# Optimization experiments

Measured on AMD Instinct MI355X. Metric: run time of the kernel, lower is better.

The kernel has to match this reference:

```python
import jax, jax.numpy as jnp
import numpy as np

D_MODEL = 768
NUM_HEADS = 12
D_K = D_MODEL // NUM_HEADS


def setup_inputs() -> dict:
    key = jax.random.key(0)
    ks = jax.random.split(key, 11)
    B, S = 2, 2048
    sc = 1.0 / np.sqrt(D_MODEL)
    return {
        "q": jax.random.normal(ks[0], (B, S, D_MODEL), jnp.float32),
        "k": jax.random.normal(ks[1], (B, S, D_MODEL), jnp.float32),
        "v": jax.random.normal(ks[2], (B, S, D_MODEL), jnp.float32),
        "w_q": jax.random.normal(ks[3], (D_MODEL, D_MODEL), jnp.float32) * sc,
        "b_q": jnp.zeros((D_MODEL,), jnp.float32),
        "w_k": jax.random.normal(ks[4], (D_MODEL, D_MODEL), jnp.float32) * sc,
        "b_k": jnp.zeros((D_MODEL,), jnp.float32),
        "w_v": jax.random.normal(ks[5], (D_MODEL, D_MODEL), jnp.float32) * sc,
        "b_v": jnp.zeros((D_MODEL,), jnp.float32),
        "w_o": jax.random.normal(ks[6], (D_MODEL, D_MODEL), jnp.float32) * sc,
        "b_o": jnp.zeros((D_MODEL,), jnp.float32),
    }


def _split_heads(x, B):
    # [B, S, D] -> [B, H, S, d_k]
    return x.reshape(B, -1, NUM_HEADS, D_K).transpose(0, 2, 1, 3)


def reference(q, k, v, w_q, b_q, w_k, b_k, w_v, b_v, w_o, b_o):
    B = q.shape[0]
    # torch nn.Linear: y = x @ W.T + b; weights stored [out, in]
    qh = _split_heads(q @ w_q.T + b_q, B)
    kh = _split_heads(k @ w_k.T + b_k, B)
    vh = _split_heads(v @ w_v.T + b_v, B)
    scores = jnp.einsum("bhsd,bhtd->bhst", qh, kh) / jnp.sqrt(jnp.float32(D_K))
    attn = jax.nn.softmax(scores, axis=-1)
    ctx = jnp.einsum("bhst,bhtd->bhsd", attn, vh)
    ctx = ctx.transpose(0, 2, 1, 3).reshape(B, -1, D_MODEL)
    return ctx @ w_o.T + b_o
```

## Files before the change

### kernel.cpp

```cpp
#include <hip/hip_runtime.h>
#include <cstdint>


#define S_LEN 2048
#define NHEAD 12
#define DMODEL 768

typedef short s16x8 __attribute__((ext_vector_type(8)));
typedef float f32x4 __attribute__((ext_vector_type(4)));

#define MFMA16(a, b, c) __builtin_amdgcn_mfma_f32_16x16x32_bf16((a), (b), (c), 0, 0, 0)

__device__ __forceinline__ unsigned int pk_bf16(float a, float b) {
  unsigned int ua = __float_as_uint(a), ub = __float_as_uint(b);
  ua = (ua + 0x7FFFu + ((ua >> 16) & 1u)) >> 16;
  ub = (ub + 0x7FFFu + ((ub >> 16) & 1u)) >> 16;
  return ua | (ub << 16);
}
__device__ __forceinline__ short bf16r(float a) {
  unsigned int ua = __float_as_uint(a);
  return (short)((ua + 0x7FFFu + ((ua >> 16) & 1u)) >> 16);
}
__device__ __forceinline__ unsigned int pk_trunc(float a, float b) {
  return __builtin_amdgcn_perm(__float_as_uint(b), __float_as_uint(a), 0x07060302u);
}
__device__ __forceinline__ float bf16_floor(float a) {
  return __uint_as_float(__float_as_uint(a) & 0xFFFF0000u);
}

__global__ __launch_bounds__(256)
void convert_w(const float* __restrict__ w0, const float* __restrict__ w1,
               const float* __restrict__ w2, const float* __restrict__ w3,
               short* __restrict__ o0, short* __restrict__ o1,
               short* __restrict__ o2, short* __restrict__ o3) {
  const float* src = (blockIdx.y == 0) ? w0 : (blockIdx.y == 1) ? w1
                   : (blockIdx.y == 2) ? w2 : w3;
  short* dst = (blockIdx.y == 0) ? o0 : (blockIdx.y == 1) ? o1
             : (blockIdx.y == 2) ? o2 : o3;
  const long i = ((long)blockIdx.x * 256 + threadIdx.x) * 4;
  float4 f = *(const float4*)(src + i);
  uint2 u;
  u.x = pk_bf16(f.x, f.y);
  u.y = pk_bf16(f.z, f.w);
  *(uint2*)(dst + i) = u;
}

template <bool ABF>
__device__ __forceinline__ void gemm64x128db(const void* __restrict__ Av,
                                             const short* __restrict__ Bv,
                                             int m0, int n0, f32x4 (&acc)[2][4],
                                             short* Alds, short* Blds) {
  constexpr int K = 768;
  constexpr int NIT = K / 32;
  const int tid  = threadIdx.x;
  const int lane = tid & 63;
  const int w    = tid >> 6;
  const int g    = lane >> 4;
  const int c    = lane & 15;
  const int wm   = (w & 1) * 32;
  const int wn   = (w >> 1) * 64;
  const int ar   = tid >> 2, ac = (tid & 3) * 8;
  const int br   = tid >> 1, bc = (tid & 1) * 16;

#pragma unroll
  for (int i = 0; i < 2; ++i)
#pragma unroll
    for (int j = 0; j < 4; ++j) acc[i][j] = (f32x4){0.f, 0.f, 0.f, 0.f};

  short* A0 = Alds;            short* B0 = Blds;
  short* A1 = Alds + 64 * 40;  short* B1 = Blds + 128 * 40;

  float4 rafA0, rafA1, rafB0, rafB1;
  uint4  rabA, rabB;
  uint4  rbA0, rbA1, rbB0, rbB1;

  auto fetchA = [&](int kt) {
    if (ABF) {
      rabA = *(const uint4*)((const short*)Av + (long)(m0 + ar) * K + kt + ac);
    } else {
      const float* Ap = (const float*)Av + (long)(m0 + ar) * K + kt + ac;
      rafA0 = ((const float4*)Ap)[0];
      rafA1 = ((const float4*)Ap)[1];
    }
    const short* Bp = Bv + (long)(n0 + br) * K + kt + bc;
    rbA0 = *(const uint4*)Bp;
    rbA1 = *(const uint4*)(Bp + 8);
  };
  auto fetchB = [&](int kt) {
    if (ABF) {
      rabB = *(const uint4*)((const short*)Av + (long)(m0 + ar) * K + kt + ac);
    } else {
      const float* Ap = (const float*)Av + (long)(m0 + ar) * K + kt + ac;
      rafB0 = ((const float4*)Ap)[0];
      rafB1 = ((const float4*)Ap)[1];
    }
    const short* Bp = Bv + (long)(n0 + br) * K + kt + bc;
    rbB0 = *(const uint4*)Bp;
    rbB1 = *(const uint4*)(Bp + 8);
  };
  auto storeA = [&](short* Ab, short* Bb) {
    if (ABF) {
      *(uint4*)&Ab[ar * 40 + ac] = rabA;
    } else {
      uint4 u;
      u.x = pk_bf16(rafA0.x, rafA0.y); u.y = pk_bf16(rafA0.z, rafA0.w);
      u.z = pk_bf16(rafA1.x, rafA1.y); u.w = pk_bf16(rafA1.z, rafA1.w);
      *(uint4*)&Ab[ar * 40 + ac] = u;
    }
    *(uint4*)&Bb[br * 40 + bc]     = rbA0;
    *(uint4*)&Bb[br * 40 + bc + 8] = rbA1;
  };
  auto storeB = [&](short* Ab, short* Bb) {
    if (ABF) {
      *(uint4*)&Ab[ar * 40 + ac] = rabB;
    } else {
      uint4 u;
      u.x = pk_bf16(rafB0.x, rafB0.y); u.y = pk_bf16(rafB0.z, rafB0.w);
      u.z = pk_bf16(rafB1.x, rafB1.y); u.w = pk_bf16(rafB1.z, rafB1.w);
      *(uint4*)&Ab[ar * 40 + ac] = u;
    }
    *(uint4*)&Bb[br * 40 + bc]     = rbB0;
    *(uint4*)&Bb[br * 40 + bc + 8] = rbB1;
  };
  auto compute = [&](const short* Ab, const short* Bb) {
    s16x8 af[2], bf[4];
#pragma unroll
    for (int mb = 0; mb < 2; ++mb)
      af[mb] = *(const s16x8*)&Ab[(wm + mb * 16 + c) * 40 + g * 8];
#pragma unroll
    for (int nb = 0; nb < 4; ++nb)
      bf[nb] = *(const s16x8*)&Bb[(wn + nb * 16 + c) * 40 + g * 8];
#pragma unroll
    for (int mb = 0; mb < 2; ++mb)
#pragma unroll
      for (int nb = 0; nb < 4; ++nb)
        acc[mb][nb] = MFMA16(af[mb], bf[nb], acc[mb][nb]);
  };

  fetchA(0);
  fetchB(32);
  storeA(A0, B0);
  for (int j = 0; j < NIT / 2; ++j) {
    __syncthreads();
    fetchA((2 * j + 2 < NIT) ? (2 * j + 2) * 32 : 0);
    compute(A0, B0);
    storeB(A1, B1);
    __syncthreads();
    fetchB((2 * j + 3 < NIT) ? (2 * j + 3) * 32 : 0);
    compute(A1, B1);
    storeA(A0, B0);
  }
}

__global__ __launch_bounds__(256)
void qkv_kernel(const float* __restrict__ q, const float* __restrict__ k,
                const float* __restrict__ v,
                const short* __restrict__ wq, const short* __restrict__ wk,
                const short* __restrict__ wv,
                const float* __restrict__ bq, const float* __restrict__ bk,
                const float* __restrict__ bv,
                short* __restrict__ qh, short* __restrict__ kh,
                short* __restrict__ vt) {
  __shared__ short Alds[2 * 64 * 40];
  __shared__ short Blds[2 * 128 * 40];

  const int L   = blockIdx.x;
  const int xcd = L & 7;
  const int i   = L >> 3;
  const int nt  = i % 6;
  const int pl  = xcd * 24 + i / 6;
  const int z   = pl >> 6;
  const int mt  = pl & 63;
  const int m0  = mt * 64;
  const int n0  = nt * 128;

  const float* A = (z == 0) ? q : (z == 1) ? k : v;
  const short* B = (z == 0) ? wq : (z == 1) ? wk : wv;
  const float* bias = (z == 0) ? bq : (z == 1) ? bk : bv;

  f32x4 acc[2][4];
  gemm64x128db<false>(A, B, m0, n0, acc, Alds, Blds);

  const int lane = threadIdx.x & 63, w = threadIdx.x >> 6;
  const int g = lane >> 4, c = lane & 15;
  const int wm = (w & 1) * 32, wn = (w >> 1) * 64;

  if (z < 2) {
    short* outp = z ? kh : qh;
    const float scale = z ? 1.0f : 0.18033688011112042f;
#pragma unroll
    for (int mb = 0; mb < 2; ++mb) {
#pragma unroll
      for (int nb = 0; nb < 4; ++nb) {
        const int n = n0 + wn + nb * 16 + c;
        const float bvv = bias[n];
        const int hh = n >> 6, d = n & 63;
#pragma unroll
        for (int r = 0; r < 4; ++r) {
          const int m = m0 + wm + mb * 16 + g * 4 + r;
          const int b = m >> 11, s = m & 2047;
          const float val = (acc[mb][nb][r] + bvv) * scale;
          outp[(((long)(b * NHEAD + hh) * S_LEN + s) << 6) + d] = bf16r(val);
        }
      }
    }
  } else {
#pragma unroll
    for (int mb = 0; mb < 2; ++mb) {
#pragma unroll
      for (int nb = 0; nb < 4; ++nb) {
        const int n = n0 + wn + nb * 16 + c;
        const float bvv = bias[n];
        const int hh = n >> 6, d = n & 63;
        const int m_base = m0 + wm + mb * 16 + g * 4;
        const int b = m_base >> 11, t = m_base & 2047;
        uint2 ov;
        ov.x = pk_bf16(acc[mb][nb][0] + bvv, acc[mb][nb][1] + bvv);
        ov.y = pk_bf16(acc[mb][nb][2] + bvv, acc[mb][nb][3] + bvv);
        *(uint2*)(vt + ((long)(b * NHEAD + hh) * 64 + d) * S_LEN + t) = ov;
      }
    }
  }
}

__global__ __launch_bounds__(256)
void o_kernel(const short* __restrict__ ctx, const short* __restrict__ wo,
              const float* __restrict__ bo, float* __restrict__ out) {
  __shared__ short Alds[2 * 64 * 40];
  __shared__ short Blds[2 * 128 * 40];

  const int L   = blockIdx.x;
  const int xcd = L & 7;
  const int i   = L >> 3;
  const int nt  = i % 6;
  const int mt  = xcd * 8 + i / 6;
  const int m0  = mt * 64;
  const int n0  = nt * 128;

  f32x4 acc[2][4];
  gemm64x128db<true>(ctx, wo, m0, n0, acc, Alds, Blds);

  const int lane = threadIdx.x & 63, w = threadIdx.x >> 6;
  const int g = lane >> 4, c = lane & 15;
  const int wm = (w & 1) * 32, wn = (w >> 1) * 64;
#pragma unroll
  for (int mb = 0; mb < 2; ++mb) {
#pragma unroll
    for (int nb = 0; nb < 4; ++nb) {
      const int n = n0 + wn + nb * 16 + c;
      const float bvv = bo[n];
#pragma unroll
      for (int r = 0; r < 4; ++r) {
        const int m = m0 + wm + mb * 16 + g * 4 + r;
        out[(long)m * DMODEL + n] = acc[mb][nb][r] + bvv;
      }
    }
  }
}

__global__ __launch_bounds__(256)
void attn_kernel(const short* __restrict__ Qh, const short* __restrict__ Kh,
                 const short* __restrict__ Vt, short* __restrict__ Ctx) {
  __shared__ short kbuf[2][64 * 64];
  __shared__ short vbuf[2][64 * 64];
  __shared__ short pbuf[4][16 * 64];

  const int tid  = threadIdx.x;
  const int lane = tid & 63;
  const int w    = tid >> 6;
  const int g    = lane >> 4;
  const int c    = lane & 15;
  const int bh   = blockIdx.y;
  const int qs0  = blockIdx.x * 64;
  const long base = (long)bh * S_LEN * 64;
  const short* Qb = Qh + base;
  const short* Kb = Kh + base;
  const short* Vb = Vt + base;

  const long qrow = (long)(qs0 + w * 16 + c) * 64;
  const s16x8 qf0 = *(const s16x8*)(Qb + qrow + g * 8);
  const s16x8 qf1 = *(const s16x8*)(Qb + qrow + 32 + g * 8);

  f32x4 co[4];
#pragma unroll
  for (int i = 0; i < 4; ++i) co[i] = (f32x4){0.f, 0.f, 0.f, 0.f};
  float l_lane = 0.f;

  const int srow = tid >> 2;
  const int sq   = tid & 3;
  const int sw   = srow & 7;
  const int sg0  = ((2 * sq)     ^ sw) * 8;
  const int sg1  = ((2 * sq + 1) ^ sw) * 8;
  const int cw   = c & 7;
  const int rg0  = ((g)     ^ cw) * 8;
  const int rg1  = ((4 + g) ^ cw) * 8;

  const short* kg = Kb + (long)srow * 64 + sq * 16;
  const short* vg = Vb + (long)srow * S_LEN + sq * 16;

  uint4 rkA0, rkA1, rvA0, rvA1;
  uint4 rkB0, rkB1, rvB0, rvB1;
  auto fetchA = [&](long t0) {
    rkA0 = *(const uint4*)(kg + t0 * 64);
    rkA1 = *(const uint4*)(kg + t0 * 64 + 8);
    rvA0 = *(const uint4*)(vg + t0);
    rvA1 = *(const uint4*)(vg + t0 + 8);
  };
  auto fetchB = [&](long t0) {
    rkB0 = *(const uint4*)(kg + t0 * 64);
    rkB1 = *(const uint4*)(kg + t0 * 64 + 8);
    rvB0 = *(const uint4*)(vg + t0);
    rvB1 = *(const uint4*)(vg + t0 + 8);
  };
  auto storeA = [&](short* kb2, short* vb2) {
    *(uint4*)&kb2[srow * 64 + sg0] = rkA0;
    *(uint4*)&kb2[srow * 64 + sg1] = rkA1;
    *(uint4*)&vb2[srow * 64 + sg0] = rvA0;
    *(uint4*)&vb2[srow * 64 + sg1] = rvA1;
  };
  auto storeB = [&](short* kb2, short* vb2) {
    *(uint4*)&kb2[srow * 64 + sg0] = rkB0;
    *(uint4*)&kb2[srow * 64 + sg1] = rkB1;
    *(uint4*)&vb2[srow * 64 + sg0] = rvB0;
    *(uint4*)&vb2[srow * 64 + sg1] = rvB1;
  };

  const int pr0 = c * 64 + ((g ^ cw) * 8);
  const int pr1 = c * 64 + (((4 + g) ^ cw) * 8);

  auto step = [&](const short* kb2, const short* vb2) {
    f32x4 st[4];
#pragma unroll
    for (int mb = 0; mb < 4; ++mb) {
      const s16x8 k0 = *(const s16x8*)&kb2[(mb * 16 + c) * 64 + rg0];
      const s16x8 k1 = *(const s16x8*)&kb2[(mb * 16 + c) * 64 + rg1];
      f32x4 z = (f32x4){0.f, 0.f, 0.f, 0.f};
      z = MFMA16(k0, qf0, z);
      z = MFMA16(k1, qf1, z);
      st[mb] = z;
    }
#pragma unroll
    for (int mb = 0; mb < 4; ++mb) {
      float p0 = __builtin_amdgcn_exp2f(st[mb][0]);
      float p1 = __builtin_amdgcn_exp2f(st[mb][1]);
      float p2 = __builtin_amdgcn_exp2f(st[mb][2]);
      float p3 = __builtin_amdgcn_exp2f(st[mb][3]);
      l_lane += bf16_floor(p0) + bf16_floor(p1) + bf16_floor(p2) + bf16_floor(p3);
      uint2 pw;
      pw.x = pk_trunc(p0, p1);
      pw.y = pk_trunc(p2, p3);
      const int pg = ((2 * mb + (g >> 1)) ^ cw) * 8 + (g & 1) * 4;
      *(uint2*)&pbuf[w][c * 64 + pg] = pw;
    }
    const s16x8 pb0 = *(const s16x8*)&pbuf[w][pr0];
    const s16x8 pb1 = *(const s16x8*)&pbuf[w][pr1];
#pragma unroll
    for (int db = 0; db < 4; ++db) {
      const s16x8 v0 = *(const s16x8*)&vb2[(db * 16 + c) * 64 + rg0];
      const s16x8 v1 = *(const s16x8*)&vb2[(db * 16 + c) * 64 + rg1];
      co[db] = MFMA16(v0, pb0, co[db]);
      co[db] = MFMA16(v1, pb1, co[db]);
    }
  };

  constexpr int NT = S_LEN / 64;
  fetchA(0);
  fetchB(64);
  storeA(kbuf[0], vbuf[0]);
  for (int j = 0; j < NT / 2; ++j) {
    __syncthreads();
    fetchA((2 * j + 2 < NT) ? (long)(2 * j + 2) * 64 : 0);
    step(kbuf[0], vbuf[0]);
    storeB(kbuf[1], vbuf[1]);
    __syncthreads();
    fetchB((2 * j + 3 < NT) ? (long)(2 * j + 3) * 64 : 0);
    step(kbuf[1], vbuf[1]);
    storeA(kbuf[0], vbuf[0]);
  }

  float rs = l_lane;
  rs += __shfl_xor(rs, 16);
  rs += __shfl_xor(rs, 32);
  const float invl = 1.f / rs;

  const int hh = bh % NHEAD;
  const long tok = (long)(bh / NHEAD) * S_LEN + qs0 + w * 16 + c;
#pragma unroll
  for (int db = 0; db < 4; ++db) {
    uint2 ov;
    ov.x = pk_bf16(co[db][0] * invl, co[db][1] * invl);
    ov.y = pk_bf16(co[db][2] * invl, co[db][3] * invl);
    *(uint2*)(Ctx + tok * DMODEL + hh * 64 + db * 16 + g * 4) = ov;
  }
}

extern "C" void kernel_launch(void* const* d_in, const int* in_sizes, int n_in,
                              void* d_out, int out_size, void* d_ws, size_t ws_size,
                              hipStream_t stream) {
  const float* q   = (const float*)d_in[0];
  const float* k   = (const float*)d_in[1];
  const float* v   = (const float*)d_in[2];
  const float* w_q = (const float*)d_in[3];
  const float* b_q = (const float*)d_in[4];
  const float* w_k = (const float*)d_in[5];
  const float* b_k = (const float*)d_in[6];
  const float* w_v = (const float*)d_in[7];
  const float* b_v = (const float*)d_in[8];
  const float* w_o = (const float*)d_in[9];
  const float* b_o = (const float*)d_in[10];
  float* out = (float*)d_out;

  const long NELEM = (long)2 * NHEAD * S_LEN * 64;
  const long WELEM = (long)DMODEL * DMODEL;
  short* qh  = (short*)d_ws;
  short* kh  = qh + NELEM;
  short* vt  = kh + NELEM;
  short* ctx = vt + NELEM;
  short* wqb = ctx + NELEM;
  short* wkb = wqb + WELEM;
  short* wvb = wkb + WELEM;
  short* wob = wvb + WELEM;

  dim3 blk(256);
  convert_w<<<dim3(576, 4), blk, 0, stream>>>(w_q, w_k, w_v, w_o,
                                              wqb, wkb, wvb, wob);
  qkv_kernel<<<dim3(1152), blk, 0, stream>>>(q, k, v, wqb, wkb, wvb,
                                             b_q, b_k, b_v, qh, kh, vt);
  attn_kernel<<<dim3(32, 24), blk, 0, stream>>>(qh, kh, vt, ctx);
  o_kernel<<<dim3(384), blk, 0, stream>>>(ctx, wob, b_o, out);
}
```

Before: 204.4 us.

## Pre-convert activations to bf16 and load GEMM MFMA fragments directly from global memory

Adds a separate kernel that converts q, k and v to bf16 in workspace before the projection GEMM. The GEMMs drop the LDS double-buffered tiling and instead load MFMA operand fragments straight from global memory into registers, with two register stages in flight. This removes LDS traffic and barriers and halves the activation bytes read inside the GEMM. In exchange it adds a full conversion pass over the activations, and each fragment row is now reloaded by several waves through cache with strided, less coalesced accesses. The ctx buffer now aliases the converted q buffer, which is no longer needed by the time attention writes it.

```diff
diff --git a/kernel.cpp b/kernel.cpp
--- a/kernel.cpp
+++ b/kernel.cpp
@@ -26,6 +26,21 @@
 }
 __device__ __forceinline__ float bf16_floor(float a) {
   return __uint_as_float(__float_as_uint(a) & 0xFFFF0000u);
+}
+
+__global__ __launch_bounds__(256)
+void convert_in(const float* __restrict__ q, const float* __restrict__ k,
+                const float* __restrict__ v,
+                short* __restrict__ qb, short* __restrict__ kb,
+                short* __restrict__ vb) {
+  const float* src = (blockIdx.y == 0) ? q : (blockIdx.y == 1) ? k : v;
+  short* dst = (blockIdx.y == 0) ? qb : (blockIdx.y == 1) ? kb : vb;
+  const long i = ((long)blockIdx.x * 256 + threadIdx.x) * 4;
+  float4 f = *(const float4*)(src + i);
+  uint2 u;
+  u.x = pk_bf16(f.x, f.y);
+  u.y = pk_bf16(f.z, f.w);
+  *(uint2*)(dst + i) = u;
 }
 
 __global__ __launch_bounds__(256)
@@ -45,125 +60,82 @@
   *(uint2*)(dst + i) = u;
 }
 
-template <bool ABF>
-__device__ __forceinline__ void gemm64x128db(const void* __restrict__ Av,
-                                             const short* __restrict__ Bv,
-                                             int m0, int n0, f32x4 (&acc)[2][4],
-                                             short* Alds, short* Blds) {
+__device__ __forceinline__ void gemm_direct(const short* __restrict__ Ab,
+                                            const short* __restrict__ Bb,
+                                            int m0, int n0, f32x4 (&acc)[2][4]) {
   constexpr int K = 768;
-  constexpr int NIT = K / 32;
-  const int tid  = threadIdx.x;
-  const int lane = tid & 63;
-  const int w    = tid >> 6;
+  const int lane = threadIdx.x & 63;
+  const int w    = threadIdx.x >> 6;
   const int g    = lane >> 4;
   const int c    = lane & 15;
   const int wm   = (w & 1) * 32;
   const int wn   = (w >> 1) * 64;
-  const int ar   = tid >> 2, ac = (tid & 3) * 8;
-  const int br   = tid >> 1, bc = (tid & 1) * 16;
 
 #pragma unroll
   for (int i = 0; i < 2; ++i)
 #pragma unroll
     for (int j = 0; j < 4; ++j) acc[i][j] = (f32x4){0.f, 0.f, 0.f, 0.f};
 
-  short* A0 = Alds;            short* B0 = Blds;
-  short* A1 = Alds + 64 * 40;  short* B1 = Blds + 128 * 40;
-
-  float4 rafA0, rafA1, rafB0, rafB1;
-  uint4  rabA, rabB;
-  uint4  rbA0, rbA1, rbB0, rbB1;
-
-  auto fetchA = [&](int kt) {
-    if (ABF) {
-      rabA = *(const uint4*)((const short*)Av + (long)(m0 + ar) * K + kt + ac);
-    } else {
-      const float* Ap = (const float*)Av + (long)(m0 + ar) * K + kt + ac;
-      rafA0 = ((const float4*)Ap)[0];
-      rafA1 = ((const float4*)Ap)[1];
-    }
-    const short* Bp = Bv + (long)(n0 + br) * K + kt + bc;
-    rbA0 = *(const uint4*)Bp;
-    rbA1 = *(const uint4*)(Bp + 8);
-  };
-  auto fetchB = [&](int kt) {
-    if (ABF) {
-      rabB = *(const uint4*)((const short*)Av + (long)(m0 + ar) * K + kt + ac);
-    } else {
-      const float* Ap = (const float*)Av + (long)(m0 + ar) * K + kt + ac;
-      rafB0 = ((const float4*)Ap)[0];
-      rafB1 = ((const float4*)Ap)[1];
-    }
-    const short* Bp = Bv + (long)(n0 + br) * K + kt + bc;
-    rbB0 = *(const uint4*)Bp;
-    rbB1 = *(const uint4*)(Bp + 8);
-  };
-  auto storeA = [&](short* Ab, short* Bb) {
-    if (ABF) {
-      *(uint4*)&Ab[ar * 40 + ac] = rabA;
-    } else {
-      uint4 u;
-      u.x = pk_bf16(rafA0.x, rafA0.y); u.y = pk_bf16(rafA0.z, rafA0.w);
-      u.z = pk_bf16(rafA1.x, rafA1.y); u.w = pk_bf16(rafA1.z, rafA1.w);
-      *(uint4*)&Ab[ar * 40 + ac] = u;
-    }
-    *(uint4*)&Bb[br * 40 + bc]     = rbA0;
-    *(uint4*)&Bb[br * 40 + bc + 8] = rbA1;
-  };
-  auto storeB = [&](short* Ab, short* Bb) {
-    if (ABF) {
-      *(uint4*)&Ab[ar * 40 + ac] = rabB;
-    } else {
-      uint4 u;
-      u.x = pk_bf16(rafB0.x, rafB0.y); u.y = pk_bf16(rafB0.z, rafB0.w);
-      u.z = pk_bf16(rafB1.x, rafB1.y); u.w = pk_bf16(rafB1.z, rafB1.w);
-      *(uint4*)&Ab[ar * 40 + ac] = u;
-    }
-    *(uint4*)&Bb[br * 40 + bc]     = rbB0;
-    *(uint4*)&Bb[br * 40 + bc + 8] = rbB1;
-  };
-  auto compute = [&](const short* Ab, const short* Bb) {
-    s16x8 af[2], bf[4];
-#pragma unroll
-    for (int mb = 0; mb < 2; ++mb)
-      af[mb] = *(const s16x8*)&Ab[(wm + mb * 16 + c) * 40 + g * 8];
-#pragma unroll
-    for (int nb = 0; nb < 4; ++nb)
-      bf[nb] = *(const s16x8*)&Bb[(wn + nb * 16 + c) * 40 + g * 8];
-#pragma unroll
-    for (int mb = 0; mb < 2; ++mb)
-#pragma unroll
-      for (int nb = 0; nb < 4; ++nb)
-        acc[mb][nb] = MFMA16(af[mb], bf[nb], acc[mb][nb]);
-  };
-
-  fetchA(0);
-  fetchB(32);
-  storeA(A0, B0);
-  for (int j = 0; j < NIT / 2; ++j) {
-    __syncthreads();
-    fetchA((2 * j + 2 < NIT) ? (2 * j + 2) * 32 : 0);
-    compute(A0, B0);
-    storeB(A1, B1);
-    __syncthreads();
-    fetchB((2 * j + 3 < NIT) ? (2 * j + 3) * 32 : 0);
-    compute(A1, B1);
-    storeA(A0, B0);
+  const short* pa0 = Ab + (long)(m0 + wm + c) * K + g * 8;
+  const short* pa1 = pa0 + 16 * K;
+  const short* pb0 = Bb + (long)(n0 + wn + c) * K + g * 8;
+  const short* pb1 = pb0 + 16 * K;
+  const short* pb2 = pb0 + 32 * K;
+  const short* pb3 = pb0 + 48 * K;
+
+  s16x8 a0A, a1A, b0A, b1A, b2A, b3A;
+  s16x8 a0B, a1B, b0B, b1B, b2B, b3B;
+
+  auto loadS0 = [&](int kt) {
+    a0A = *(const s16x8*)(pa0 + kt); a1A = *(const s16x8*)(pa1 + kt);
+    b0A = *(const s16x8*)(pb0 + kt); b1A = *(const s16x8*)(pb1 + kt);
+    b2A = *(const s16x8*)(pb2 + kt); b3A = *(const s16x8*)(pb3 + kt);
+  };
+  auto loadS1 = [&](int kt) {
+    a0B = *(const s16x8*)(pa0 + kt); a1B = *(const s16x8*)(pa1 + kt);
+    b0B = *(const s16x8*)(pb0 + kt); b1B = *(const s16x8*)(pb1 + kt);
+    b2B = *(const s16x8*)(pb2 + kt); b3B = *(const s16x8*)(pb3 + kt);
+  };
+  auto mfmaS0 = [&]() {
+    acc[0][0] = MFMA16(a0A, b0A, acc[0][0]);
+    acc[0][1] = MFMA16(a0A, b1A, acc[0][1]);
+    acc[0][2] = MFMA16(a0A, b2A, acc[0][2]);
+    acc[0][3] = MFMA16(a0A, b3A, acc[0][3]);
+    acc[1][0] = MFMA16(a1A, b0A, acc[1][0]);
+    acc[1][1] = MFMA16(a1A, b1A, acc[1][1]);
+    acc[1][2] = MFMA16(a1A, b2A, acc[1][2]);
+    acc[1][3] = MFMA16(a1A, b3A, acc[1][3]);
+  };
+  auto mfmaS1 = [&]() {
+    acc[0][0] = MFMA16(a0B, b0B, acc[0][0]);
+    acc[0][1] = MFMA16(a0B, b1B, acc[0][1]);
+    acc[0][2] = MFMA16(a0B, b2B, acc[0][2]);
+    acc[0][3] = MFMA16(a0B, b3B, acc[0][3]);
+    acc[1][0] = MFMA16(a1B, b0B, acc[1][0]);
+    acc[1][1] = MFMA16(a1B, b1B, acc[1][1]);
+    acc[1][2] = MFMA16(a1B, b2B, acc[1][2]);
+    acc[1][3] = MFMA16(a1B, b3B, acc[1][3]);
+  };
+
+  loadS0(0);
+#pragma unroll
+  for (int j = 0; j < 12; ++j) {
+    loadS1(j * 64 + 32);
+    mfmaS0();
+    loadS0(j * 64 + 64 < K ? j * 64 + 64 : 0);
+    mfmaS1();
   }
 }
 
 __global__ __launch_bounds__(256)
-void qkv_kernel(const float* __restrict__ q, const float* __restrict__ k,
-                const float* __restrict__ v,
+void qkv_kernel(const short* __restrict__ qb, const short* __restrict__ kb,
+                const short* __restrict__ vb,
                 const short* __restrict__ wq, const short* __restrict__ wk,
                 const short* __restrict__ wv,
                 const float* __restrict__ bq, const float* __restrict__ bk,
                 const float* __restrict__ bv,
                 short* __restrict__ qh, short* __restrict__ kh,
                 short* __restrict__ vt) {
-  __shared__ short Alds[2 * 64 * 40];
-  __shared__ short Blds[2 * 128 * 40];
-
   const int L   = blockIdx.x;
   const int xcd = L & 7;
   const int i   = L >> 3;
@@ -174,12 +146,12 @@
   const int m0  = mt * 64;
   const int n0  = nt * 128;
 
-  const float* A = (z == 0) ? q : (z == 1) ? k : v;
+  const short* A = (z == 0) ? qb : (z == 1) ? kb : vb;
   const short* B = (z == 0) ? wq : (z == 1) ? wk : wv;
   const float* bias = (z == 0) ? bq : (z == 1) ? bk : bv;
 
   f32x4 acc[2][4];
-  gemm64x128db<false>(A, B, m0, n0, acc, Alds, Blds);
+  gemm_direct(A, B, m0, n0, acc);
 
   const int lane = threadIdx.x & 63, w = threadIdx.x >> 6;
   const int g = lane >> 4, c = lane & 15;
@@ -226,9 +198,6 @@
 __global__ __launch_bounds__(256)
 void o_kernel(const short* __restrict__ ctx, const short* __restrict__ wo,
               const float* __restrict__ bo, float* __restrict__ out) {
-  __shared__ short Alds[2 * 64 * 40];
-  __shared__ short Blds[2 * 128 * 40];
-
   const int L   = blockIdx.x;
   const int xcd = L & 7;
   const int i   = L >> 3;
@@ -238,7 +207,7 @@
   const int n0  = nt * 128;
 
   f32x4 acc[2][4];
-  gemm64x128db<true>(ctx, wo, m0, n0, acc, Alds, Blds);
+  gemm_direct(ctx, wo, m0, n0, acc);
 
   const int lane = threadIdx.x & 63, w = threadIdx.x >> 6;
   const int g = lane >> 4, c = lane & 15;
@@ -415,16 +384,20 @@
   short* qh  = (short*)d_ws;
   short* kh  = qh + NELEM;
   short* vt  = kh + NELEM;
-  short* ctx = vt + NELEM;
-  short* wqb = ctx + NELEM;
+  short* wqb = vt + NELEM;
   short* wkb = wqb + WELEM;
   short* wvb = wkb + WELEM;
   short* wob = wvb + WELEM;
+  short* qb  = wob + WELEM;
+  short* kb  = qb + NELEM;
+  short* vb  = kb + NELEM;
+  short* ctx = qb;
 
   dim3 blk(256);
+  convert_in<<<dim3(3072, 3), blk, 0, stream>>>(q, k, v, qb, kb, vb);
   convert_w<<<dim3(576, 4), blk, 0, stream>>>(w_q, w_k, w_v, w_o,
                                               wqb, wkb, wvb, wob);
-  qkv_kernel<<<dim3(1152), blk, 0, stream>>>(q, k, v, wqb, wkb, wvb,
+  qkv_kernel<<<dim3(1152), blk, 0, stream>>>(qb, kb, vb, wqb, wkb, wvb,
                                              b_q, b_k, b_v, qh, kh, vt);
   attn_kernel<<<dim3(32, 24), blk, 0, stream>>>(qh, kh, vt, ctx);
   o_kernel<<<dim3(384), blk, 0, stream>>>(ctx, wob, b_o, out);
```

Result: slower. 265.5 us (+29.9%).
